# Kernel tuning notes

Measured on AMD Instinct MI355X. Metric: run time of the kernel, lower is better.

Reference implementation:

```python
import jax, jax.numpy as jnp
import numpy as np

N_NODES = 100000
N_EDGES = 640000
NIN = 128
NOUT = 128


def setup_inputs() -> dict:
    key = jax.random.key(0)
    ks = jax.random.split(key, 10)
    scale = 1.0 / np.sqrt(NIN)
    x = jax.random.normal(ks[0], (N_NODES, NIN), dtype=jnp.float32)
    edge_index = jax.random.randint(ks[1], (2, N_EDGES), 0, N_NODES, dtype=jnp.int64)
    edge_attr = jnp.zeros((N_EDGES, 1), dtype=jnp.float32)
    Wk = jax.random.uniform(ks[2], (NIN, NOUT), jnp.float32, -scale, scale)
    bk = jax.random.uniform(ks[3], (NOUT,), jnp.float32, -scale, scale)
    Wq = jax.random.uniform(ks[4], (NIN, NOUT), jnp.float32, -scale, scale)
    bq = jax.random.uniform(ks[5], (NOUT,), jnp.float32, -scale, scale)
    Wv = jax.random.uniform(ks[6], (NIN, NOUT), jnp.float32, -scale, scale)
    bv = jax.random.uniform(ks[7], (NOUT,), jnp.float32, -scale, scale)
    Wskip = jax.random.uniform(ks[8], (NIN, NOUT), jnp.float32, -scale, scale)
    bias = jax.random.uniform(ks[9], (NOUT,), jnp.float32, -scale, scale)
    return {
        "x": x, "edge_index": edge_index, "edge_attr": edge_attr,
        "Wk": Wk, "bk": bk, "Wq": Wq, "bq": bq,
        "Wv": Wv, "bv": bv, "Wskip": Wskip, "bias": bias,
    }


def reference(x, edge_index, edge_attr, Wk, bk, Wq, bq, Wv, bv, Wskip, bias):
    # PyG ResGatedGraphConv: out_i = W_skip x_i + b + sum_{j->i} sigmoid(k_i + q_j) * v_j
    # k = lin_key(x) (applied to dst), q = lin_query(x) (src), v = lin_value(x) (src)
    src, dst = edge_index[0], edge_index[1]
    k = x @ Wk + bk            # [N, NOUT]
    q = x @ Wq + bq            # [N, NOUT]
    v = x @ Wv + bv            # [N, NOUT]
    eta = jax.nn.sigmoid(k[dst] + q[src])   # [E, NOUT] per-edge gate
    msg = eta * v[src]                       # [E, NOUT]
    agg = jax.ops.segment_sum(msg, dst, num_segments=x.shape[0])  # [N, NOUT]
    return agg + x @ Wskip + bias
```

## Files before the change

kernel.cpp:

```cpp
#include <hip/hip_runtime.h>
#include <hip/hip_bf16.h>

typedef __bf16 v4bf __attribute__((ext_vector_type(4)));
typedef __bf16 v8bf __attribute__((ext_vector_type(8)));
typedef float  v16f __attribute__((ext_vector_type(16)));
typedef float  f4v  __attribute__((ext_vector_type(4)));
typedef unsigned int u4v __attribute__((ext_vector_type(4)));

#define LOG2E 1.44269504088896340736f

__device__ __forceinline__ unsigned short f2bf(float f) {
    union { float f; unsigned int u; } a; a.f = f;
    unsigned int r = a.u + 0x7FFFu + ((a.u >> 16) & 1u);
    return (unsigned short)(r >> 16);
}

__device__ __forceinline__ void unpack8v(u4v w, float* f) {
    #pragma unroll
    for (int i = 0; i < 4; ++i) {
        f[2 * i]     = __uint_as_float(w[i] << 16);
        f[2 * i + 1] = __uint_as_float(w[i] & 0xFFFF0000u);
    }
}

__global__ __launch_bounds__(256) void prep_w_zero(
    const float* __restrict__ Wk, const float* __restrict__ Wq,
    const float* __restrict__ Wv, const float* __restrict__ Ws,
    unsigned short* __restrict__ Wt, int* __restrict__ deg, int N)
{
    int i = blockIdx.x * 256 + threadIdx.x;
    if (i < 65536) {
        int m = i >> 14;
        int r = i & 16383;
        int n = r >> 7, k = r & 127;
        const float* W = (m == 0) ? Wk : (m == 1) ? Wq : (m == 2) ? Wv : Ws;
        float scale = (m == 0) ? -LOG2E : (m == 1) ? LOG2E : 1.0f;
        Wt[i] = f2bf(W[k * 128 + n] * scale);
    }
    if (i < N) deg[i] = 0;
}

__global__ __launch_bounds__(1024, 4) void gemm_fused(
    const float* __restrict__ x, int N,
    const unsigned short* __restrict__ Wt,
    const float* __restrict__ bk, const float* __restrict__ bq,
    const float* __restrict__ bv, const float* __restrict__ bs,
    unsigned short* __restrict__ kws, unsigned short* __restrict__ qv,
    float* __restrict__ out)
{
    __shared__ __align__(16) unsigned short xs[32 * 132];
    const int t   = threadIdx.x;
    const int wid = t >> 6;
    const int m   = wid >> 2;
    const int ct  = wid & 3;
    const int l   = t & 63;
    const int col = ct * 32 + (l & 31);
    const int kb  = (l >> 5) * 8;

    v8bf b[8];
    {
        const unsigned short* wp = Wt + m * 16384 + col * 128 + kb;
        #pragma unroll
        for (int c = 0; c < 8; ++c) b[c] = *(const v8bf*)(wp + c * 16);
    }
    const float* bvec = (m == 0) ? bk : (m == 1) ? bq : (m == 2) ? bv : bs;
    const float bcol = bvec[col] * ((m == 0) ? -LOG2E : (m == 1) ? LOG2E : 1.0f);
    unsigned short* dst; int dstride;
    if (m == 0)      { dst = kws;      dstride = 128; }
    else if (m == 1) { dst = qv;       dstride = 256; }
    else             { dst = qv + 128; dstride = 256; }

    const int srow = t >> 5;
    const int sk4  = (t & 31) << 2;
    const int rowb = 4 * (l >> 5);

    const int ntiles = (N + 31) >> 5;
    int tile = blockIdx.x;
    if (tile >= ntiles) return;

    float4 stg = make_float4(0.f, 0.f, 0.f, 0.f);
    {
        int gr = tile * 32 + srow;
        if (gr < N) stg = *(const float4*)(x + (size_t)gr * 128 + sk4);
    }

    const unsigned short* ap = xs + (l & 31) * 132 + kb;

    while (true) {
        ushort4 pk;
        pk.x = f2bf(stg.x); pk.y = f2bf(stg.y);
        pk.z = f2bf(stg.z); pk.w = f2bf(stg.w);
        *(ushort4*)(xs + srow * 132 + sk4) = pk;
        __syncthreads();

        int next = tile + gridDim.x;
        if (next < ntiles) {
            int gr = next * 32 + srow;
            stg = (gr < N) ? *(const float4*)(x + (size_t)gr * 128 + sk4)
                           : make_float4(0.f, 0.f, 0.f, 0.f);
        }

        v16f acc = {};
        #pragma unroll
        for (int c = 0; c < 8; ++c) {
            v4bf a0 = *(const v4bf*)(ap + c * 16);
            v4bf a1 = *(const v4bf*)(ap + c * 16 + 4);
            v8bf a = __builtin_shufflevector(a0, a1, 0, 1, 2, 3, 4, 5, 6, 7);
            acc = __builtin_amdgcn_mfma_f32_32x32x16_bf16(a, b[c], acc, 0, 0, 0);
        }

        const int r0 = tile * 32 + rowb;
        if (m == 3) {
            #pragma unroll
            for (int reg = 0; reg < 16; ++reg) {
                int row = r0 + (reg & 3) + 8 * (reg >> 2);
                if (row < N) out[(size_t)row * 128 + col] = acc[reg] + bcol;
            }
        } else {
            #pragma unroll
            for (int reg = 0; reg < 16; ++reg) {
                int row = r0 + (reg & 3) + 8 * (reg >> 2);
                if (row < N) dst[(size_t)row * dstride + col] = f2bf(acc[reg] + bcol);
            }
        }

        tile = next;
        if (tile >= ntiles) break;
        __syncthreads();
    }
}


__global__ __launch_bounds__(256) void count_pos(
    const int* __restrict__ ei, int E, int* __restrict__ deg,
    int* __restrict__ pos)
{
    int e = blockIdx.x * 256 + threadIdx.x;
    if (e >= E) return;
    pos[e] = atomicAdd(&deg[ei[E + e]], 1);
}

__global__ __launch_bounds__(256) void scan_chunks(
    const int* __restrict__ deg, int N, int* __restrict__ rowStart,
    int* __restrict__ chunkTot)
{
    __shared__ int sums[256];
    const int t = threadIdx.x;
    const int base = blockIdx.x * 1024 + t * 4;
    int d0 = 0, d1 = 0, d2 = 0, d3 = 0;
    if (base + 3 < N) {
        int4 dd = *(const int4*)(deg + base);
        d0 = dd.x; d1 = dd.y; d2 = dd.z; d3 = dd.w;
    } else {
        if (base + 0 < N) d0 = deg[base + 0];
        if (base + 1 < N) d1 = deg[base + 1];
        if (base + 2 < N) d2 = deg[base + 2];
        if (base + 3 < N) d3 = deg[base + 3];
    }
    int tot = d0 + d1 + d2 + d3;
    sums[t] = tot;
    __syncthreads();
    #pragma unroll
    for (int off = 1; off < 256; off <<= 1) {
        int v = (t >= off) ? sums[t - off] : 0;
        __syncthreads();
        sums[t] += v;
        __syncthreads();
    }
    int excl = sums[t] - tot;
    if (base + 0 < N) rowStart[base + 0] = excl;
    if (base + 1 < N) rowStart[base + 1] = excl + d0;
    if (base + 2 < N) rowStart[base + 2] = excl + d0 + d1;
    if (base + 3 < N) rowStart[base + 3] = excl + d0 + d1 + d2;
    if (t == 255) chunkTot[blockIdx.x] = sums[255];
}

__global__ __launch_bounds__(256) void add_offsets(
    int* __restrict__ rowStart, const int* __restrict__ chunkTot,
    int N, int nChunks)
{
    __shared__ int s[128];
    const int t = threadIdx.x;
    if (t < 128) s[t] = (t < nChunks) ? chunkTot[t] : 0;
    __syncthreads();
    #pragma unroll
    for (int off = 1; off < 128; off <<= 1) {
        int u = 0;
        if (t < 128 && t >= off) u = s[t - off];
        __syncthreads();
        if (t < 128) s[t] += u;
        __syncthreads();
    }
    const int coff = (blockIdx.x == 0) ? 0 : s[blockIdx.x - 1];
    const int base = blockIdx.x * 1024 + t * 4;
    if (base + 3 < N) {
        int4 r = *(const int4*)(rowStart + base);
        r.x += coff; r.y += coff; r.z += coff; r.w += coff;
        *(int4*)(rowStart + base) = r;
    } else {
        #pragma unroll
        for (int j = 0; j < 4; ++j) {
            if (base + j < N) rowStart[base + j] += coff;
        }
    }
}

__global__ __launch_bounds__(256) void fill_csr(
    const int* __restrict__ ei, int E,
    const int* __restrict__ rowStart, const int* __restrict__ pos,
    int* __restrict__ elist)
{
    int e = blockIdx.x * 256 + threadIdx.x;
    if (e >= E) return;
    int s = ei[e];
    int d = ei[E + e];
    elist[rowStart[d] + pos[e]] = s;
}

__global__ __launch_bounds__(256, 4) void gather_agg(
    const int* __restrict__ rowStart, const int* __restrict__ deg,
    const int* __restrict__ elist,
    const unsigned short* __restrict__ kws,
    const unsigned short* __restrict__ qv,
    float* __restrict__ out, int N)
{
    int gid = blockIdx.x * 256 + threadIdx.x;
    int node = gid >> 4;
    if (node >= N) return;
    int fo = (gid & 15) << 3;

    float* orow = out + (size_t)node * 128 + fo;
    f4v o0 = __builtin_nontemporal_load((const f4v*)orow);
    f4v o1 = __builtin_nontemporal_load((const f4v*)(orow + 4));
    u4v kraw = __builtin_nontemporal_load((const u4v*)(kws + (size_t)node * 128 + fo));
    const int p0 = rowStart[node];
    const int dg = deg[node];

    float nkf[8];
    unpack8v(kraw, nkf);
    float acc[8] = {};

    const unsigned short* qvb = qv + fo;
    const int e = p0 + dg;

    if (dg > 0) {
        u4v qA[4], vA[4], qB[4], vB[4];

#define LOADC(b, qr, vr)                                                     \
        {                                                                    \
            _Pragma("unroll")                                                \
            for (int s = 0; s < 4; ++s) {                                    \
                int pp = (b) + s;                                            \
                int ix = __builtin_nontemporal_load(elist + (pp < e ? pp : e - 1)); \
                const unsigned short* r = qvb + (ix << 8);                   \
                qr[s] = *(const u4v*)(r);                                    \
                vr[s] = *(const u4v*)(r + 128);                              \
            }                                                                \
        }

#define COMP(b, qr, vr)                                                     \
        {                                                                   \
            _Pragma("unroll")                                               \
            for (int s = 0; s < 4; ++s) {                                   \
                u4v vv = vr[s];                                             \
                if ((b) + s >= e) { vv[0]=0u; vv[1]=0u; vv[2]=0u; vv[3]=0u; } \
                float qf[8], vf[8];                                         \
                unpack8v(qr[s], qf);                                        \
                unpack8v(vv, vf);                                           \
                _Pragma("unroll")                                           \
                for (int j = 0; j < 8; ++j) {                               \
                    float ex = __builtin_amdgcn_exp2f(nkf[j] - qf[j]);      \
                    acc[j] = fmaf(__builtin_amdgcn_rcpf(1.0f + ex), vf[j], acc[j]); \
                }                                                           \
            }                                                               \
        }

        int base = p0;
        LOADC(base, qA, vA);
        while (true) {
            int nb = base + 4;
            if (nb < e) {
                LOADC(nb, qB, vB);
                COMP(base, qA, vA);
                base = nb;
                nb = base + 4;
                if (nb < e) {
                    LOADC(nb, qA, vA);
                    COMP(base, qB, vB);
                    base = nb;
                } else {
                    COMP(base, qB, vB);
                    break;
                }
            } else {
                COMP(base, qA, vA);
                break;
            }
        }
#undef LOADC
#undef COMP
    }

    o0[0] += acc[0]; o0[1] += acc[1]; o0[2] += acc[2]; o0[3] += acc[3];
    o1[0] += acc[4]; o1[1] += acc[5]; o1[2] += acc[6]; o1[3] += acc[7];
    __builtin_nontemporal_store(o0, (f4v*)orow);
    __builtin_nontemporal_store(o1, (f4v*)(orow + 4));
}

extern "C" void kernel_launch(void* const* d_in, const int* in_sizes, int n_in,
                              void* d_out, int out_size, void* d_ws, size_t ws_size,
                              hipStream_t stream) {
    const float* x    = (const float*)d_in[0];
    const int*   ei   = (const int*)d_in[1];
    const float* Wk   = (const float*)d_in[3];
    const float* bk   = (const float*)d_in[4];
    const float* Wq   = (const float*)d_in[5];
    const float* bq   = (const float*)d_in[6];
    const float* Wv   = (const float*)d_in[7];
    const float* bv   = (const float*)d_in[8];
    const float* Ws   = (const float*)d_in[9];
    const float* bias = (const float*)d_in[10];

    const int N = in_sizes[0] / 128;
    const int E = in_sizes[1] / 2;
    float* out = (float*)d_out;

    unsigned short* kws = (unsigned short*)d_ws;
    unsigned short* qv  = kws + (size_t)N * 128;
    int* deg      = (int*)(qv + (size_t)N * 256);
    int* rowStart = deg + N;
    int* chunkTot = rowStart + N;
    int* pos      = chunkTot + 128;
    int* elist    = pos + E;
    unsigned short* Wt = (unsigned short*)(elist + E);

    const int nChunks = (N + 1023) / 1024;

    prep_w_zero<<<512, 256, 0, stream>>>(Wk, Wq, Wv, Ws, Wt, deg, N);
    gemm_fused<<<1024, 1024, 0, stream>>>(
        x, N, Wt, bk, bq, bv, bias, kws, qv, out);

    count_pos<<<(E + 255) / 256, 256, 0, stream>>>(ei, E, deg, pos);
    scan_chunks<<<nChunks, 256, 0, stream>>>(deg, N, rowStart, chunkTot);
    add_offsets<<<nChunks, 256, 0, stream>>>(rowStart, chunkTot, N, nChunks);
    fill_csr<<<(E + 255) / 256, 256, 0, stream>>>(ei, E, rowStart, pos, elist);

    gather_agg<<<((size_t)N * 16 + 255) / 256, 256, 0, stream>>>(
        rowStart, deg, elist, kws, qv, out, N);
}
```

Baseline: 285.0 us.

## Sort nodes by in-degree before gather to balance wavefront work

Builds a degree histogram during the scan, computes descending bin offsets, and scatters node ids into a degree-sorted permutation. The gather kernel then processes nodes in that order, so the 16-thread groups sharing a wavefront have similar edge counts and less divergence, with high-degree nodes scheduled first. It also replaces nontemporal loads and stores with plain ones. The cost is an extra kernel launch, more atomics, and scattered rather than sequential writes to the output rows.

```diff
diff --git a/kernel.cpp b/kernel.cpp
--- a/kernel.cpp
+++ b/kernel.cpp
@@ -8,6 +8,7 @@
 typedef unsigned int u4v __attribute__((ext_vector_type(4)));
 
 #define LOG2E 1.44269504088896340736f
+#define NBIN 64
 
 __device__ __forceinline__ unsigned short f2bf(float f) {
     union { float f; unsigned int u; } a; a.f = f;
@@ -26,7 +27,8 @@
 __global__ __launch_bounds__(256) void prep_w_zero(
     const float* __restrict__ Wk, const float* __restrict__ Wq,
     const float* __restrict__ Wv, const float* __restrict__ Ws,
-    unsigned short* __restrict__ Wt, int* __restrict__ deg, int N)
+    unsigned short* __restrict__ Wt, int* __restrict__ deg,
+    int* __restrict__ hist, int* __restrict__ binCnt, int N)
 {
     int i = blockIdx.x * 256 + threadIdx.x;
     if (i < 65536) {
@@ -38,6 +40,7 @@
         Wt[i] = f2bf(W[k * 128 + n] * scale);
     }
     if (i < N) deg[i] = 0;
+    if (i < NBIN) { hist[i] = 0; binCnt[i] = 0; }
 }
 
 __global__ __launch_bounds__(1024, 4) void gemm_fused(
@@ -142,10 +145,12 @@
 
 __global__ __launch_bounds__(256) void scan_chunks(
     const int* __restrict__ deg, int N, int* __restrict__ rowStart,
-    int* __restrict__ chunkTot)
+    int* __restrict__ chunkTot, int* __restrict__ hist)
 {
     __shared__ int sums[256];
+    __shared__ int h[NBIN];
     const int t = threadIdx.x;
+    if (t < NBIN) h[t] = 0;
     const int base = blockIdx.x * 1024 + t * 4;
     int d0 = 0, d1 = 0, d2 = 0, d3 = 0;
     if (base + 3 < N) {
@@ -160,6 +165,10 @@
     int tot = d0 + d1 + d2 + d3;
     sums[t] = tot;
     __syncthreads();
+    if (base + 0 < N) atomicAdd(&h[min(d0, NBIN - 1)], 1);
+    if (base + 1 < N) atomicAdd(&h[min(d1, NBIN - 1)], 1);
+    if (base + 2 < N) atomicAdd(&h[min(d2, NBIN - 1)], 1);
+    if (base + 3 < N) atomicAdd(&h[min(d3, NBIN - 1)], 1);
     #pragma unroll
     for (int off = 1; off < 256; off <<= 1) {
         int v = (t >= off) ? sums[t - off] : 0;
@@ -173,10 +182,12 @@
     if (base + 2 < N) rowStart[base + 2] = excl + d0 + d1;
     if (base + 3 < N) rowStart[base + 3] = excl + d0 + d1 + d2;
     if (t == 255) chunkTot[blockIdx.x] = sums[255];
+    if (t < NBIN && h[t] > 0) atomicAdd(&hist[t], h[t]);
 }
 
 __global__ __launch_bounds__(256) void add_offsets(
     int* __restrict__ rowStart, const int* __restrict__ chunkTot,
+    const int* __restrict__ hist, int* __restrict__ binStart,
     int N, int nChunks)
 {
     __shared__ int s[128];
@@ -203,6 +214,10 @@
             if (base + j < N) rowStart[base + j] += coff;
         }
     }
+    if (blockIdx.x == 0 && t == 0) {
+        int run = 0;
+        for (int b = NBIN - 1; b >= 0; --b) { binStart[b] = run; run += hist[b]; }
+    }
 }
 
 __global__ __launch_bounds__(256) void fill_csr(
@@ -217,7 +232,29 @@
     elist[rowStart[d] + pos[e]] = s;
 }
 
+__global__ __launch_bounds__(256) void scatter_perm(
+    const int* __restrict__ deg, int N, const int* __restrict__ binStart,
+    int* __restrict__ binCnt, int* __restrict__ perm)
+{
+    __shared__ int h[NBIN];
+    __shared__ int sbase[NBIN];
+    const int t = threadIdx.x;
+    if (t < NBIN) h[t] = 0;
+    __syncthreads();
+    int i = blockIdx.x * 256 + t;
+    int b = 0, rank = 0;
+    if (i < N) {
+        b = min(deg[i], NBIN - 1);
+        rank = atomicAdd(&h[b], 1);
+    }
+    __syncthreads();
+    if (t < NBIN && h[t] > 0) sbase[t] = atomicAdd(&binCnt[t], h[t]);
+    __syncthreads();
+    if (i < N) perm[binStart[b] + sbase[b] + rank] = i;
+}
+
 __global__ __launch_bounds__(256, 4) void gather_agg(
+    const int* __restrict__ perm,
     const int* __restrict__ rowStart, const int* __restrict__ deg,
     const int* __restrict__ elist,
     const unsigned short* __restrict__ kws,
@@ -225,14 +262,15 @@
     float* __restrict__ out, int N)
 {
     int gid = blockIdx.x * 256 + threadIdx.x;
-    int node = gid >> 4;
-    if (node >= N) return;
+    int ni = gid >> 4;
+    if (ni >= N) return;
+    const int node = perm[ni];
     int fo = (gid & 15) << 3;
 
     float* orow = out + (size_t)node * 128 + fo;
-    f4v o0 = __builtin_nontemporal_load((const f4v*)orow);
-    f4v o1 = __builtin_nontemporal_load((const f4v*)(orow + 4));
-    u4v kraw = __builtin_nontemporal_load((const u4v*)(kws + (size_t)node * 128 + fo));
+    f4v o0 = *(const f4v*)(orow);
+    f4v o1 = *(const f4v*)(orow + 4);
+    u4v kraw = *(const u4v*)(kws + (size_t)node * 128 + fo);
     const int p0 = rowStart[node];
     const int dg = deg[node];
 
@@ -251,7 +289,7 @@
             _Pragma("unroll")                                                \
             for (int s = 0; s < 4; ++s) {                                    \
                 int pp = (b) + s;                                            \
-                int ix = __builtin_nontemporal_load(elist + (pp < e ? pp : e - 1)); \
+                int ix = elist[pp < e ? pp : e - 1];                         \
                 const unsigned short* r = qvb + (ix << 8);                   \
                 qr[s] = *(const u4v*)(r);                                    \
                 vr[s] = *(const u4v*)(r + 128);                              \
@@ -303,8 +341,8 @@
 
     o0[0] += acc[0]; o0[1] += acc[1]; o0[2] += acc[2]; o0[3] += acc[3];
     o1[0] += acc[4]; o1[1] += acc[5]; o1[2] += acc[6]; o1[3] += acc[7];
-    __builtin_nontemporal_store(o0, (f4v*)orow);
-    __builtin_nontemporal_store(o1, (f4v*)(orow + 4));
+    *(f4v*)(orow)     = o0;
+    *(f4v*)(orow + 4) = o1;
 }
 
 extern "C" void kernel_launch(void* const* d_in, const int* in_sizes, int n_in,
@@ -332,19 +370,24 @@
     int* chunkTot = rowStart + N;
     int* pos      = chunkTot + 128;
     int* elist    = pos + E;
-    unsigned short* Wt = (unsigned short*)(elist + E);
+    int* perm     = elist + E;
+    int* hist     = perm + N;
+    int* binStart = hist + NBIN;
+    int* binCnt   = binStart + NBIN;
+    unsigned short* Wt = (unsigned short*)(binCnt + NBIN);
 
     const int nChunks = (N + 1023) / 1024;
 
-    prep_w_zero<<<512, 256, 0, stream>>>(Wk, Wq, Wv, Ws, Wt, deg, N);
+    prep_w_zero<<<512, 256, 0, stream>>>(Wk, Wq, Wv, Ws, Wt, deg, hist, binCnt, N);
     gemm_fused<<<1024, 1024, 0, stream>>>(
         x, N, Wt, bk, bq, bv, bias, kws, qv, out);
 
     count_pos<<<(E + 255) / 256, 256, 0, stream>>>(ei, E, deg, pos);
-    scan_chunks<<<nChunks, 256, 0, stream>>>(deg, N, rowStart, chunkTot);
-    add_offsets<<<nChunks, 256, 0, stream>>>(rowStart, chunkTot, N, nChunks);
+    scan_chunks<<<nChunks, 256, 0, stream>>>(deg, N, rowStart, chunkTot, hist);
+    add_offsets<<<nChunks, 256, 0, stream>>>(rowStart, chunkTot, hist, binStart, N, nChunks);
     fill_csr<<<(E + 255) / 256, 256, 0, stream>>>(ei, E, rowStart, pos, elist);
+    scatter_perm<<<(N + 255) / 256, 256, 0, stream>>>(deg, N, binStart, binCnt, perm);
 
     gather_agg<<<((size_t)N * 16 + 255) / 256, 256, 0, stream>>>(
-        rowStart, deg, elist, kws, qv, out, N);
-}
+        perm, rowStart, deg, elist, kws, qv, out, N);
+}
```

Result: slower. 290.8 us (+2.0%).

## Sort nodes by degree within blocks to balance gather work across wavefronts

Applied to the files above, without the earlier changes.

Folds a per-256-node degree bucketing into the CSR fill kernel, producing a permutation that groups nodes of similar in-degree inside each block. The gather kernel then processes nodes in permuted order so the 16-lane node groups sharing a wavefront have similar loop trip counts, which cuts divergence. It also drops the nontemporal load and store hints and moves the output read after the edge loop. The cost is an extra indirection, less sequential output access, and losing the cache hints.

```diff
diff --git a/kernel.cpp b/kernel.cpp
--- a/kernel.cpp
+++ b/kernel.cpp
@@ -8,6 +8,7 @@
 typedef unsigned int u4v __attribute__((ext_vector_type(4)));
 
 #define LOG2E 1.44269504088896340736f
+#define NBIN 64
 
 __device__ __forceinline__ unsigned short f2bf(float f) {
     union { float f; unsigned int u; } a; a.f = f;
@@ -205,19 +206,51 @@
     }
 }
 
-__global__ __launch_bounds__(256) void fill_csr(
+__global__ __launch_bounds__(256) void fill_csr_perm(
     const int* __restrict__ ei, int E,
     const int* __restrict__ rowStart, const int* __restrict__ pos,
-    int* __restrict__ elist)
-{
-    int e = blockIdx.x * 256 + threadIdx.x;
-    if (e >= E) return;
-    int s = ei[e];
-    int d = ei[E + e];
-    elist[rowStart[d] + pos[e]] = s;
+    int* __restrict__ elist,
+    const int* __restrict__ deg, int N, int* __restrict__ perm)
+{
+    __shared__ int h[NBIN];
+    __shared__ int boff[NBIN];
+    const int t = threadIdx.x;
+    const int nbase = blockIdx.x * 256;
+
+    if (nbase < N) {
+        if (t < NBIN) h[t] = 0;
+        __syncthreads();
+        int i = nbase + t;
+        int bin = 0, rank = 0;
+        if (i < N) {
+            bin = min(deg[i], NBIN - 1);
+            rank = atomicAdd(&h[bin], 1);
+        }
+        __syncthreads();
+        if (t < NBIN) {
+            int v = h[t];
+            int inc = v;
+            #pragma unroll
+            for (int off = 1; off < NBIN; off <<= 1) {
+                int u = __shfl_up(inc, off);
+                if ((t & 63) >= off) inc += u;
+            }
+            boff[t] = inc - v;
+        }
+        __syncthreads();
+        if (i < N) perm[nbase + boff[bin] + rank] = i;
+    }
+
+    int e = nbase + t;
+    if (e < E) {
+        int s = ei[e];
+        int d = ei[E + e];
+        elist[rowStart[d] + pos[e]] = s;
+    }
 }
 
 __global__ __launch_bounds__(256, 4) void gather_agg(
+    const int* __restrict__ perm,
     const int* __restrict__ rowStart, const int* __restrict__ deg,
     const int* __restrict__ elist,
     const unsigned short* __restrict__ kws,
@@ -225,14 +258,12 @@
     float* __restrict__ out, int N)
 {
     int gid = blockIdx.x * 256 + threadIdx.x;
-    int node = gid >> 4;
-    if (node >= N) return;
+    int ni = gid >> 4;
+    if (ni >= N) return;
+    const int node = perm[ni];
     int fo = (gid & 15) << 3;
 
-    float* orow = out + (size_t)node * 128 + fo;
-    f4v o0 = __builtin_nontemporal_load((const f4v*)orow);
-    f4v o1 = __builtin_nontemporal_load((const f4v*)(orow + 4));
-    u4v kraw = __builtin_nontemporal_load((const u4v*)(kws + (size_t)node * 128 + fo));
+    u4v kraw = *(const u4v*)(kws + (size_t)node * 128 + fo);
     const int p0 = rowStart[node];
     const int dg = deg[node];
 
@@ -251,7 +282,7 @@
             _Pragma("unroll")                                                \
             for (int s = 0; s < 4; ++s) {                                    \
                 int pp = (b) + s;                                            \
-                int ix = __builtin_nontemporal_load(elist + (pp < e ? pp : e - 1)); \
+                int ix = elist[pp < e ? pp : e - 1];                         \
                 const unsigned short* r = qvb + (ix << 8);                   \
                 qr[s] = *(const u4v*)(r);                                    \
                 vr[s] = *(const u4v*)(r + 128);                              \
@@ -301,10 +332,13 @@
 #undef COMP
     }
 
+    float* orow = out + (size_t)node * 128 + fo;
+    f4v o0 = *(const f4v*)(orow);
+    f4v o1 = *(const f4v*)(orow + 4);
     o0[0] += acc[0]; o0[1] += acc[1]; o0[2] += acc[2]; o0[3] += acc[3];
     o1[0] += acc[4]; o1[1] += acc[5]; o1[2] += acc[6]; o1[3] += acc[7];
-    __builtin_nontemporal_store(o0, (f4v*)orow);
-    __builtin_nontemporal_store(o1, (f4v*)(orow + 4));
+    *(f4v*)(orow)     = o0;
+    *(f4v*)(orow + 4) = o1;
 }
 
 extern "C" void kernel_launch(void* const* d_in, const int* in_sizes, int n_in,
@@ -332,7 +366,8 @@
     int* chunkTot = rowStart + N;
     int* pos      = chunkTot + 128;
     int* elist    = pos + E;
-    unsigned short* Wt = (unsigned short*)(elist + E);
+    int* perm     = elist + E;
+    unsigned short* Wt = (unsigned short*)(perm + N);
 
     const int nChunks = (N + 1023) / 1024;
 
@@ -343,8 +378,9 @@
     count_pos<<<(E + 255) / 256, 256, 0, stream>>>(ei, E, deg, pos);
     scan_chunks<<<nChunks, 256, 0, stream>>>(deg, N, rowStart, chunkTot);
     add_offsets<<<nChunks, 256, 0, stream>>>(rowStart, chunkTot, N, nChunks);
-    fill_csr<<<(E + 255) / 256, 256, 0, stream>>>(ei, E, rowStart, pos, elist);
+    fill_csr_perm<<<(E + 255) / 256, 256, 0, stream>>>(
+        ei, E, rowStart, pos, elist, deg, N, perm);
 
     gather_agg<<<((size_t)N * 16 + 255) / 256, 256, 0, stream>>>(
-        rowStart, deg, elist, kws, qv, out, N);
-}
+        perm, rowStart, deg, elist, kws, qv, out, N);
+}
```

Result: no change. 281.0 us (-1.4%).
